# Kernel tuning notes

Measured on AMD Instinct MI355X. Metric: run time of the kernel, lower is better.

The kernel has to match this reference:

```python
import jax, jax.numpy as jnp
import numpy as np

B, S, EMBED = 8, 2048, 512
FFN = 2048
N_QUBITS = 10
DEPTH = 2


def _apply_1q(state, mats, wire):
    # state: (N,) + (2,)*n complex; mats: (N,2,2) per-token or (2,2) shared
    s = jnp.moveaxis(state, 1 + wire, 1)
    shp = s.shape
    s = s.reshape(shp[0], 2, -1)
    if mats.ndim == 3:
        s = jnp.einsum('nab,nbr->nar', mats, s)
    else:
        s = jnp.einsum('ab,nbr->nar', mats, s)
    return jnp.moveaxis(s.reshape(shp), 1, 1 + wire)


def _cnot(state, ctrl, tgt):
    # CNOT: flip target axis on the control=1 slice
    ca, ta = 1 + ctrl, 1 + tgt
    s0 = jax.lax.index_in_dim(state, 0, axis=ca, keepdims=True)
    s1 = jax.lax.index_in_dim(state, 1, axis=ca, keepdims=True)
    s1 = jnp.flip(s1, axis=ta)
    return jnp.concatenate([s0, s1], axis=ca)


def _qlayer(x_flat, theta, n_qubits=N_QUBITS, depth=DEPTH):
    # x_flat: (N, n_qubits) RX encoding angles; theta: (n_qubits,) RY params
    N = x_flat.shape[0]
    state = jnp.zeros((N,) + (2,) * n_qubits, jnp.complex64)
    state = state.at[(slice(None),) + (0,) * n_qubits].set(1.0)
    # encoder: RX(x_i) on wire i, per-token angles
    for w in range(n_qubits):
        a = x_flat[:, w] * 0.5
        c = jnp.cos(a).astype(jnp.complex64)
        s = (-1j * jnp.sin(a)).astype(jnp.complex64)
        mats = jnp.stack([jnp.stack([c, s], -1), jnp.stack([s, c], -1)], -2)  # (N,2,2)
        state = _apply_1q(state, mats, w)
    # trainable RY(theta_w) on each wire (shared across tokens)
    for w in range(n_qubits):
        a = theta[w] * 0.5
        c, s = jnp.cos(a), jnp.sin(a)
        mat = jnp.stack([jnp.stack([c, -s]), jnp.stack([s, c])]).astype(jnp.complex64)
        state = _apply_1q(state, mat, w)
    # depth rounds of ring CNOT chain
    for _ in range(depth):
        for w in range(n_qubits - 1):
            state = _cnot(state, w, w + 1)
        state = _cnot(state, n_qubits - 1, 0)
    # MeasureAll PauliZ: <Z_w> per wire
    probs = jnp.abs(state.reshape(N, -1)) ** 2  # (N, 2^n)
    bits = (jnp.arange(2 ** n_qubits)[None, :] >> (n_qubits - 1 - jnp.arange(n_qubits))[:, None]) & 1
    z = (1 - 2 * bits).astype(probs.dtype)  # (n, 2^n)
    return probs @ z.T  # (N, n)


def setup_inputs() -> dict:
    key = jax.random.key(0)
    k = jax.random.split(key, 6)
    x = jax.random.normal(k[0], (B, S, EMBED), jnp.float32)
    ry_theta = jax.random.uniform(k[1], (N_QUBITS,), jnp.float32, 0.0, 2.0 * np.pi)
    W1 = jax.random.normal(k[2], (FFN, N_QUBITS), jnp.float32) / np.sqrt(N_QUBITS)
    b1 = jax.random.normal(k[3], (FFN,), jnp.float32) * 0.01
    W2 = jax.random.normal(k[4], (EMBED, FFN), jnp.float32) / np.sqrt(FFN)
    b2 = jax.random.normal(k[5], (EMBED,), jnp.float32) * 0.01
    return {"x": x, "ry_theta": ry_theta, "W1": W1, "b1": b1, "W2": W2, "b2": b2}


def reference(x, ry_theta, W1, b1, W2, b2):
    b, s, _ = x.shape
    xf = x.reshape(b * s, -1)[:, :N_QUBITS]  # encoder only uses first n_qubits feats
    q = _qlayer(xf, ry_theta).reshape(b, s, N_QUBITS)
    # dropout is identity at eval; linear1 -> relu -> linear2
    h = jax.nn.relu(q @ W1.T + b1)
    return h @ W2.T + b2
```

## Files before the change

### kernel.cpp

```cpp
#include <hip/hip_runtime.h>
#include <hip/hip_bf16.h>


typedef __attribute__((ext_vector_type(8))) short bf16x8;
typedef __attribute__((ext_vector_type(16))) float f32x16;
typedef __attribute__((ext_vector_type(8))) unsigned short us8;
typedef unsigned int u32;

#define NTOK  16384
#define EMBED 512
#define FFN   2048
#define NQ    10
#define BM    128
#define BN    128
#define NKT   32

__device__ __forceinline__ unsigned short f2bf(float f) {
  union { float f; unsigned int u; } a; a.f = f;
  unsigned int r = a.u + 0x7FFFu + ((a.u >> 16) & 1u);
  return (unsigned short)(r >> 16);
}

__device__ __forceinline__ void gload_lds16(const void* g, void* l) {
  __builtin_amdgcn_global_load_lds(
      (const __attribute__((address_space(1))) unsigned int*)g,
      (__attribute__((address_space(3))) unsigned int*)l, 16, 0, 0);
}

__global__ __launch_bounds__(256) void k_prep(const float* __restrict__ x,
                                              const float* __restrict__ theta,
                                              const float* __restrict__ W1,
                                              const float* __restrict__ b1,
                                              const float* __restrict__ W2,
                                              unsigned short* __restrict__ W2f,
                                              unsigned short* __restrict__ W1f,
                                              unsigned short* __restrict__ Qf) {
  int bb = blockIdx.x;
  if (bb < 512) {
    int gid = bb * 256 + threadIdx.x;
    int l = gid & 63, kb = (gid >> 6) & 127, tile = gid >> 13;
    int col = tile * 32 + (l & 31);
    int k0 = kb * 16 + (l >> 5) * 8;
    const float* src = W2 + (size_t)col * FFN + k0;
    float4 v0 = *(const float4*)src;
    float4 v1 = *(const float4*)(src + 4);
    us8 o;
    o[0] = f2bf(v0.x); o[1] = f2bf(v0.y); o[2] = f2bf(v0.z); o[3] = f2bf(v0.w);
    o[4] = f2bf(v1.x); o[5] = f2bf(v1.y); o[6] = f2bf(v1.z); o[7] = f2bf(v1.w);
    *(us8*)(W2f + (size_t)gid * 8) = o;
  } else if (bb < 640) {
    int gid = (bb - 512) * 256 + threadIdx.x;
    int l = gid & 63, tile = gid >> 6;
    int tok = tile * 32 + (l & 31), g = l >> 5;
    const int masks[NQ] = {0x2AB,0x3FD,0x3FA,0x3F5,0x3EA,0x3D5,0x3AA,0x355,0x2AA,0x155};
    float z[NQ], qv[NQ];
#pragma unroll
    for (int w = 0; w < NQ; ++w)
      z[w] = __builtin_cosf(x[(size_t)tok * EMBED + w]) * __builtin_cosf(theta[w]);
#pragma unroll
    for (int w = 0; w < NQ; ++w) {
      float p = 1.f;
#pragma unroll
      for (int v = 0; v < NQ; ++v)
        if ((masks[w] >> v) & 1) p *= z[v];
      qv[w] = p;
    }
    us8 o = (us8)0;
    if (g == 0) {
#pragma unroll
      for (int e = 0; e < 8; ++e) o[e] = f2bf(qv[e]);
    } else {
      o[0] = f2bf(qv[8]); o[1] = f2bf(qv[9]); o[2] = f2bf(1.f);
    }
    *(us8*)(Qf + (size_t)gid * 8) = o;
  } else {
    int gid = (bb - 640) * 256 + threadIdx.x;
    int l = gid & 63, blk = gid >> 6;
    int k = blk * 32 + (l & 31);
    int wg = (l >> 5) * 8;
    us8 o;
#pragma unroll
    for (int e = 0; e < 8; ++e) {
      int wire = wg + e;
      float v = (wire < NQ) ? W1[k * NQ + wire] : (wire == NQ ? b1[k] : 0.f);
      o[e] = f2bf(v);
    }
    *(us8*)(W1f + (size_t)gid * 8) = o;
  }
}

__global__ __launch_bounds__(512, 4) void k_fused(const unsigned short* __restrict__ Qf,
                                                  const unsigned short* __restrict__ W1f,
                                                  const unsigned short* __restrict__ W2f,
                                                  const float* __restrict__ b2,
                                                  float* __restrict__ out) {
  __shared__ short Bw[2][16 * 64 * 8];
  __shared__ short W1s[2][2 * 64 * 8];

  int bid = blockIdx.x;
  int swz = (bid & 7) * 64 + (bid >> 3);
  const int m0 = (swz >> 2) * BM;
  const int n0 = (swz & 3) * BN;
  const int tid  = threadIdx.x;
  const int lane = tid & 63;
  const int wave = tid >> 6;
  const int wm = wave >> 1, wn = wave & 1;
  const int h = lane >> 5, t31 = lane & 31;
  const int nt0 = n0 >> 5;

  bf16x8 qf = *(const bf16x8*)&Qf[(((size_t)(m0 >> 5) + wm) * 64 + lane) * 8];

  f32x16 acc[2] = {};

#define STAGE(KT, B)                                                            \
  { _Pragma("unroll")                                                           \
    for (int hf = 0; hf < 2; ++hf) {                                            \
      int ch = hf * 512 + tid;                                                  \
      int tile2 = ch >> 8, kb = (ch >> 6) & 3, ln = ch & 63;                    \
      gload_lds16(&W2f[(((size_t)(nt0 + tile2) * 128 + (KT) * 4 + kb) * 64 + ln) * 8], \
                  &Bw[B][ch * 8]);                                              \
    }                                                                           \
    if (tid < 128)                                                              \
      gload_lds16(&W1f[(((size_t)(KT) * 2 + (tid >> 6)) * 64 + (tid & 63)) * 8],\
                  &W1s[B][tid * 8]); }

#define HGEN1(WF, AQ0, AQ1)                                                     \
  { f32x16 zz = {};                                                             \
    f32x16 d = __builtin_amdgcn_mfma_f32_32x32x16_bf16((WF), qf, zz, 0, 0, 0);  \
    u32 dw0, dw1, dw2, dw3, dw4, dw5, dw6, dw7;                                 \
    { float a0=fmaxf(d[0],0.f),a1=fmaxf(d[1],0.f);                              \
      asm("v_cvt_pk_bf16_f32 %0, %1, %2":"=v"(dw0):"v"(a0),"v"(a1)); }          \
    { float a0=fmaxf(d[2],0.f),a1=fmaxf(d[3],0.f);                              \
      asm("v_cvt_pk_bf16_f32 %0, %1, %2":"=v"(dw1):"v"(a0),"v"(a1)); }          \
    { float a0=fmaxf(d[4],0.f),a1=fmaxf(d[5],0.f);                              \
      asm("v_cvt_pk_bf16_f32 %0, %1, %2":"=v"(dw2):"v"(a0),"v"(a1)); }          \
    { float a0=fmaxf(d[6],0.f),a1=fmaxf(d[7],0.f);                              \
      asm("v_cvt_pk_bf16_f32 %0, %1, %2":"=v"(dw3):"v"(a0),"v"(a1)); }          \
    { float a0=fmaxf(d[8],0.f),a1=fmaxf(d[9],0.f);                              \
      asm("v_cvt_pk_bf16_f32 %0, %1, %2":"=v"(dw4):"v"(a0),"v"(a1)); }          \
    { float a0=fmaxf(d[10],0.f),a1=fmaxf(d[11],0.f);                            \
      asm("v_cvt_pk_bf16_f32 %0, %1, %2":"=v"(dw5):"v"(a0),"v"(a1)); }          \
    { float a0=fmaxf(d[12],0.f),a1=fmaxf(d[13],0.f);                            \
      asm("v_cvt_pk_bf16_f32 %0, %1, %2":"=v"(dw6):"v"(a0),"v"(a1)); }          \
    { float a0=fmaxf(d[14],0.f),a1=fmaxf(d[15],0.f);                            \
      asm("v_cvt_pk_bf16_f32 %0, %1, %2":"=v"(dw7):"v"(a0),"v"(a1)); }          \
    asm("v_permlane32_swap_b32 %0, %1" : "+v"(dw0), "+v"(dw2));                 \
    asm("v_permlane32_swap_b32 %0, %1" : "+v"(dw1), "+v"(dw3));                 \
    asm("v_permlane32_swap_b32 %0, %1" : "+v"(dw4), "+v"(dw6));                 \
    asm("v_permlane32_swap_b32 %0, %1" : "+v"(dw5), "+v"(dw7));                 \
    union { u32 u[4]; bf16x8 v; } u0, u1;                                       \
    u0.u[0]=dw0; u0.u[1]=dw1; u0.u[2]=dw2; u0.u[3]=dw3;                         \
    u1.u[0]=dw4; u1.u[1]=dw5; u1.u[2]=dw6; u1.u[3]=dw7;                         \
    AQ0 = u0.v; AQ1 = u1.v; }

  STAGE(0, 0);

  for (int kt = 0; kt < NKT; ++kt) {
    const int cur = kt & 1;
    asm volatile("s_waitcnt vmcnt(0)" ::: "memory");
    __builtin_amdgcn_s_barrier();
    asm volatile("" ::: "memory");
    if (kt + 1 < NKT) STAGE(kt + 1, cur ^ 1);

    bf16x8 wf0 = *(const bf16x8*)&W1s[cur][(0 * 64 + lane) * 8];
    bf16x8 wf1 = *(const bf16x8*)&W1s[cur][(1 * 64 + lane) * 8];
    bf16x8 aq00, aq01, aq10, aq11;
    HGEN1(wf0, aq00, aq01);
    HGEN1(wf1, aq10, aq11);

#pragma unroll
    for (int j = 0; j < 2; ++j) {
      bf16x8 bg0 = *(const bf16x8*)&Bw[cur][(((wn * 2 + j) * 4 + 0) * 64 + lane) * 8];
      bf16x8 bg1 = *(const bf16x8*)&Bw[cur][(((wn * 2 + j) * 4 + 1) * 64 + lane) * 8];
      bf16x8 bg2 = *(const bf16x8*)&Bw[cur][(((wn * 2 + j) * 4 + 2) * 64 + lane) * 8];
      bf16x8 bg3 = *(const bf16x8*)&Bw[cur][(((wn * 2 + j) * 4 + 3) * 64 + lane) * 8];
      __builtin_amdgcn_s_setprio(1);
      acc[j] = __builtin_amdgcn_mfma_f32_32x32x16_bf16(aq00, bg0, acc[j], 0, 0, 0);
      acc[j] = __builtin_amdgcn_mfma_f32_32x32x16_bf16(aq01, bg1, acc[j], 0, 0, 0);
      acc[j] = __builtin_amdgcn_mfma_f32_32x32x16_bf16(aq10, bg2, acc[j], 0, 0, 0);
      acc[j] = __builtin_amdgcn_mfma_f32_32x32x16_bf16(aq11, bg3, acc[j], 0, 0, 0);
      __builtin_amdgcn_s_setprio(0);
    }
  }

#pragma unroll
  for (int j = 0; j < 2; ++j) {
    const int col = n0 + wn * 64 + j * 32 + t31;
    const float bbv = b2[col];
#pragma unroll
    for (int r = 0; r < 16; ++r) {
      int tok = m0 + wm * 32 + (r & 3) + 8 * (r >> 2) + 4 * h;
      out[(size_t)tok * EMBED + col] = acc[j][r] + bbv;
    }
  }
#undef STAGE
#undef HGEN1
}

extern "C" void kernel_launch(void* const* d_in, const int* in_sizes, int n_in,
                              void* d_out, int out_size, void* d_ws, size_t ws_size,
                              hipStream_t stream) {
  const float* x     = (const float*)d_in[0];
  const float* theta = (const float*)d_in[1];
  const float* W1    = (const float*)d_in[2];
  const float* b1    = (const float*)d_in[3];
  const float* W2    = (const float*)d_in[4];
  const float* b2    = (const float*)d_in[5];
  float* out = (float*)d_out;

  char* ws = (char*)d_ws;
  unsigned short* W2f = (unsigned short*)ws;
  unsigned short* W1f = (unsigned short*)(ws + (2u << 20));
  unsigned short* Qfg = (unsigned short*)(ws + (2u << 20) + (64u << 10));

  k_prep <<<656, 256, 0, stream>>>(x, theta, W1, b1, W2, W2f, W1f, Qfg);
  k_fused<<<(NTOK / BM) * (EMBED / BN), 512, 0, stream>>>(Qfg, W1f, W2f, b2, out);
}
```

Before: 57.44 us.

## Double K-step per barrier, read W1 fragments from global, vectorize ReLU

Each LDS stage now covers two K-tiles (64 of the FFN dimension) instead of one, so barriers and waitcnt drains happen half as often, and the loop is unrolled over buffers. W1 fragments are no longer staged through LDS; each wave loads them straight from global memory, relying on cache hits. The ReLU is applied as one vector max before the bf16 packing. The cost is double the LDS footprint (64KB per block), which may reduce occupancy against the launch bound of 4 blocks, plus exposed global-load latency for W1 right after the barrier.

New measurement: 59.36 us. +3.3%, slower.

```diff
diff --git a/kernel.cpp b/kernel.cpp
--- a/kernel.cpp
+++ b/kernel.cpp
@@ -13,7 +13,7 @@
 #define NQ    10
 #define BM    128
 #define BN    128
-#define NKT   32
+#define NPAIR 16
 
 __device__ __forceinline__ unsigned short f2bf(float f) {
   union { float f; unsigned int u; } a; a.f = f;
@@ -94,8 +94,7 @@
                                                   const unsigned short* __restrict__ W2f,
                                                   const float* __restrict__ b2,
                                                   float* __restrict__ out) {
-  __shared__ short Bw[2][16 * 64 * 8];
-  __shared__ short W1s[2][2 * 64 * 8];
+  __shared__ short Bw[2][32 * 64 * 8];
 
   int bid = blockIdx.x;
   int swz = (bid & 7) * 64 + (bid >> 3);
@@ -112,38 +111,28 @@
 
   f32x16 acc[2] = {};
 
-#define STAGE(KT, B)                                                            \
+#define STAGE(P, B)                                                             \
   { _Pragma("unroll")                                                           \
-    for (int hf = 0; hf < 2; ++hf) {                                            \
+    for (int hf = 0; hf < 4; ++hf) {                                            \
       int ch = hf * 512 + tid;                                                  \
-      int tile2 = ch >> 8, kb = (ch >> 6) & 3, ln = ch & 63;                    \
-      gload_lds16(&W2f[(((size_t)(nt0 + tile2) * 128 + (KT) * 4 + kb) * 64 + ln) * 8], \
+      int tile2 = ch >> 9, kbl = (ch >> 6) & 7, ln = ch & 63;                   \
+      gload_lds16(&W2f[(((size_t)(nt0 + tile2) * 128 + (P) * 8 + kbl) * 64 + ln) * 8], \
                   &Bw[B][ch * 8]);                                              \
-    }                                                                           \
-    if (tid < 128)                                                              \
-      gload_lds16(&W1f[(((size_t)(KT) * 2 + (tid >> 6)) * 64 + (tid & 63)) * 8],\
-                  &W1s[B][tid * 8]); }
+    } }
 
 #define HGEN1(WF, AQ0, AQ1)                                                     \
   { f32x16 zz = {};                                                             \
     f32x16 d = __builtin_amdgcn_mfma_f32_32x32x16_bf16((WF), qf, zz, 0, 0, 0);  \
+    d = __builtin_elementwise_max(d, zz);                                       \
     u32 dw0, dw1, dw2, dw3, dw4, dw5, dw6, dw7;                                 \
-    { float a0=fmaxf(d[0],0.f),a1=fmaxf(d[1],0.f);                              \
-      asm("v_cvt_pk_bf16_f32 %0, %1, %2":"=v"(dw0):"v"(a0),"v"(a1)); }          \
-    { float a0=fmaxf(d[2],0.f),a1=fmaxf(d[3],0.f);                              \
-      asm("v_cvt_pk_bf16_f32 %0, %1, %2":"=v"(dw1):"v"(a0),"v"(a1)); }          \
-    { float a0=fmaxf(d[4],0.f),a1=fmaxf(d[5],0.f);                              \
-      asm("v_cvt_pk_bf16_f32 %0, %1, %2":"=v"(dw2):"v"(a0),"v"(a1)); }          \
-    { float a0=fmaxf(d[6],0.f),a1=fmaxf(d[7],0.f);                              \
-      asm("v_cvt_pk_bf16_f32 %0, %1, %2":"=v"(dw3):"v"(a0),"v"(a1)); }          \
-    { float a0=fmaxf(d[8],0.f),a1=fmaxf(d[9],0.f);                              \
-      asm("v_cvt_pk_bf16_f32 %0, %1, %2":"=v"(dw4):"v"(a0),"v"(a1)); }          \
-    { float a0=fmaxf(d[10],0.f),a1=fmaxf(d[11],0.f);                            \
-      asm("v_cvt_pk_bf16_f32 %0, %1, %2":"=v"(dw5):"v"(a0),"v"(a1)); }          \
-    { float a0=fmaxf(d[12],0.f),a1=fmaxf(d[13],0.f);                            \
-      asm("v_cvt_pk_bf16_f32 %0, %1, %2":"=v"(dw6):"v"(a0),"v"(a1)); }          \
-    { float a0=fmaxf(d[14],0.f),a1=fmaxf(d[15],0.f);                            \
-      asm("v_cvt_pk_bf16_f32 %0, %1, %2":"=v"(dw7):"v"(a0),"v"(a1)); }          \
+    asm("v_cvt_pk_bf16_f32 %0, %1, %2":"=v"(dw0):"v"(d[0]),"v"(d[1]));          \
+    asm("v_cvt_pk_bf16_f32 %0, %1, %2":"=v"(dw1):"v"(d[2]),"v"(d[3]));          \
+    asm("v_cvt_pk_bf16_f32 %0, %1, %2":"=v"(dw2):"v"(d[4]),"v"(d[5]));          \
+    asm("v_cvt_pk_bf16_f32 %0, %1, %2":"=v"(dw3):"v"(d[6]),"v"(d[7]));          \
+    asm("v_cvt_pk_bf16_f32 %0, %1, %2":"=v"(dw4):"v"(d[8]),"v"(d[9]));          \
+    asm("v_cvt_pk_bf16_f32 %0, %1, %2":"=v"(dw5):"v"(d[10]),"v"(d[11]));        \
+    asm("v_cvt_pk_bf16_f32 %0, %1, %2":"=v"(dw6):"v"(d[12]),"v"(d[13]));        \
+    asm("v_cvt_pk_bf16_f32 %0, %1, %2":"=v"(dw7):"v"(d[14]),"v"(d[15]));        \
     asm("v_permlane32_swap_b32 %0, %1" : "+v"(dw0), "+v"(dw2));                 \
     asm("v_permlane32_swap_b32 %0, %1" : "+v"(dw1), "+v"(dw3));                 \
     asm("v_permlane32_swap_b32 %0, %1" : "+v"(dw4), "+v"(dw6));                 \
@@ -153,34 +142,43 @@
     u1.u[0]=dw4; u1.u[1]=dw5; u1.u[2]=dw6; u1.u[3]=dw7;                         \
     AQ0 = u0.v; AQ1 = u1.v; }
 
+#define KTBODY(Q, B, WFA, WFB)                                                  \
+  { bf16x8 aq00, aq01, aq10, aq11;                                              \
+    HGEN1(WFA, aq00, aq01);                                                     \
+    HGEN1(WFB, aq10, aq11);                                                     \
+    _Pragma("unroll")                                                           \
+    for (int j = 0; j < 2; ++j) {                                               \
+      bf16x8 bg0 = *(const bf16x8*)&Bw[B][(((wn * 2 + j) * 8 + (Q) * 4 + 0) * 64 + lane) * 8]; \
+      bf16x8 bg1 = *(const bf16x8*)&Bw[B][(((wn * 2 + j) * 8 + (Q) * 4 + 1) * 64 + lane) * 8]; \
+      bf16x8 bg2 = *(const bf16x8*)&Bw[B][(((wn * 2 + j) * 8 + (Q) * 4 + 2) * 64 + lane) * 8]; \
+      bf16x8 bg3 = *(const bf16x8*)&Bw[B][(((wn * 2 + j) * 8 + (Q) * 4 + 3) * 64 + lane) * 8]; \
+      __builtin_amdgcn_s_setprio(1);                                            \
+      acc[j] = __builtin_amdgcn_mfma_f32_32x32x16_bf16(aq00, bg0, acc[j], 0, 0, 0); \
+      acc[j] = __builtin_amdgcn_mfma_f32_32x32x16_bf16(aq01, bg1, acc[j], 0, 0, 0); \
+      acc[j] = __builtin_amdgcn_mfma_f32_32x32x16_bf16(aq10, bg2, acc[j], 0, 0, 0); \
+      acc[j] = __builtin_amdgcn_mfma_f32_32x32x16_bf16(aq11, bg3, acc[j], 0, 0, 0); \
+      __builtin_amdgcn_s_setprio(0);                                            \
+    } }
+
+#define PAIR(P, B)                                                              \
+  {                                                                             \
+    asm volatile("s_waitcnt vmcnt(0)" ::: "memory");       \
+    __builtin_amdgcn_s_barrier();                       \
+    asm volatile("" ::: "memory");                                              \
+    bf16x8 wf0 = *(const bf16x8*)&W1f[(((size_t)(P) * 4 + 0) * 64 + lane) * 8]; \
+    bf16x8 wf1 = *(const bf16x8*)&W1f[(((size_t)(P) * 4 + 1) * 64 + lane) * 8]; \
+    bf16x8 wf2 = *(const bf16x8*)&W1f[(((size_t)(P) * 4 + 2) * 64 + lane) * 8]; \
+    bf16x8 wf3 = *(const bf16x8*)&W1f[(((size_t)(P) * 4 + 3) * 64 + lane) * 8]; \
+    if ((P) + 1 < NPAIR) STAGE((P) + 1, (B) ^ 1);                               \
+    KTBODY(0, B, wf0, wf1);                                                     \
+    KTBODY(1, B, wf2, wf3);                                                     \
+  }
+
   STAGE(0, 0);
 
-  for (int kt = 0; kt < NKT; ++kt) {
-    const int cur = kt & 1;
-    asm volatile("s_waitcnt vmcnt(0)" ::: "memory");
-    __builtin_amdgcn_s_barrier();
-    asm volatile("" ::: "memory");
-    if (kt + 1 < NKT) STAGE(kt + 1, cur ^ 1);
-
-    bf16x8 wf0 = *(const bf16x8*)&W1s[cur][(0 * 64 + lane) * 8];
-    bf16x8 wf1 = *(const bf16x8*)&W1s[cur][(1 * 64 + lane) * 8];
-    bf16x8 aq00, aq01, aq10, aq11;
-    HGEN1(wf0, aq00, aq01);
-    HGEN1(wf1, aq10, aq11);
-
-#pragma unroll
-    for (int j = 0; j < 2; ++j) {
-      bf16x8 bg0 = *(const bf16x8*)&Bw[cur][(((wn * 2 + j) * 4 + 0) * 64 + lane) * 8];
-      bf16x8 bg1 = *(const bf16x8*)&Bw[cur][(((wn * 2 + j) * 4 + 1) * 64 + lane) * 8];
-      bf16x8 bg2 = *(const bf16x8*)&Bw[cur][(((wn * 2 + j) * 4 + 2) * 64 + lane) * 8];
-      bf16x8 bg3 = *(const bf16x8*)&Bw[cur][(((wn * 2 + j) * 4 + 3) * 64 + lane) * 8];
-      __builtin_amdgcn_s_setprio(1);
-      acc[j] = __builtin_amdgcn_mfma_f32_32x32x16_bf16(aq00, bg0, acc[j], 0, 0, 0);
-      acc[j] = __builtin_amdgcn_mfma_f32_32x32x16_bf16(aq01, bg1, acc[j], 0, 0, 0);
-      acc[j] = __builtin_amdgcn_mfma_f32_32x32x16_bf16(aq10, bg2, acc[j], 0, 0, 0);
-      acc[j] = __builtin_amdgcn_mfma_f32_32x32x16_bf16(aq11, bg3, acc[j], 0, 0, 0);
-      __builtin_amdgcn_s_setprio(0);
-    }
+  for (int p2 = 0; p2 < NPAIR / 2; ++p2) {
+    PAIR(2 * p2,     0);
+    PAIR(2 * p2 + 1, 1);
   }
 
 #pragma unroll
@@ -195,6 +193,8 @@
   }
 #undef STAGE
 #undef HGEN1
+#undef KTBODY
+#undef PAIR
 }
 
 extern "C" void kernel_launch(void* const* d_in, const int* in_sizes, int n_in,
```

## Halve block N-tile and workgroup size, interleave MFMA accumulators

Applied to the files above, without the earlier changes.

Shrinks the N tile from 128 to 64 and the workgroup from 8 to 4 waves, so each wave covers one 32-row M slice and both 32-column N subtiles. The grid doubles to 1024 blocks, giving more parallelism and smaller LDS per block. The MFMA chain interleaves two independent accumulators to hide dependency latency, drops the setprio hints, and applies ReLU as a single vector max. The tradeoff is more blocks each loading their own W1/W2 slices, and hidden-layer generation repeated across more n-tiles.

New measurement: 55.67 us, median of 3. -3.1%, faster.

```diff
diff --git a/kernel.cpp b/kernel.cpp
--- a/kernel.cpp
+++ b/kernel.cpp
@@ -12,7 +12,7 @@
 #define FFN   2048
 #define NQ    10
 #define BM    128
-#define BN    128
+#define BN    64
 #define NKT   32
 
 __device__ __forceinline__ unsigned short f2bf(float f) {
@@ -89,33 +89,32 @@
   }
 }
 
-__global__ __launch_bounds__(512, 4) void k_fused(const unsigned short* __restrict__ Qf,
+__global__ __launch_bounds__(256, 4) void k_fused(const unsigned short* __restrict__ Qf,
                                                   const unsigned short* __restrict__ W1f,
                                                   const unsigned short* __restrict__ W2f,
                                                   const float* __restrict__ b2,
                                                   float* __restrict__ out) {
-  __shared__ short Bw[2][16 * 64 * 8];
+  __shared__ short Bw[2][8 * 64 * 8];
   __shared__ short W1s[2][2 * 64 * 8];
 
   int bid = blockIdx.x;
-  int swz = (bid & 7) * 64 + (bid >> 3);
-  const int m0 = (swz >> 2) * BM;
-  const int n0 = (swz & 3) * BN;
+  int swz = (bid & 7) * 128 + (bid >> 3);
+  const int m0 = (swz >> 3) * BM;
+  const int n0 = (swz & 7) * BN;
   const int tid  = threadIdx.x;
   const int lane = tid & 63;
   const int wave = tid >> 6;
-  const int wm = wave >> 1, wn = wave & 1;
   const int h = lane >> 5, t31 = lane & 31;
   const int nt0 = n0 >> 5;
 
-  bf16x8 qf = *(const bf16x8*)&Qf[(((size_t)(m0 >> 5) + wm) * 64 + lane) * 8];
+  bf16x8 qf = *(const bf16x8*)&Qf[(((size_t)(m0 >> 5) + wave) * 64 + lane) * 8];
 
   f32x16 acc[2] = {};
 
 #define STAGE(KT, B)                                                            \
   { _Pragma("unroll")                                                           \
     for (int hf = 0; hf < 2; ++hf) {                                            \
-      int ch = hf * 512 + tid;                                                  \
+      int ch = hf * 256 + tid;                                                  \
       int tile2 = ch >> 8, kb = (ch >> 6) & 3, ln = ch & 63;                    \
       gload_lds16(&W2f[(((size_t)(nt0 + tile2) * 128 + (KT) * 4 + kb) * 64 + ln) * 8], \
                   &Bw[B][ch * 8]);                                              \
@@ -127,23 +126,16 @@
 #define HGEN1(WF, AQ0, AQ1)                                                     \
   { f32x16 zz = {};                                                             \
     f32x16 d = __builtin_amdgcn_mfma_f32_32x32x16_bf16((WF), qf, zz, 0, 0, 0);  \
+    d = __builtin_elementwise_max(d, zz);                                       \
     u32 dw0, dw1, dw2, dw3, dw4, dw5, dw6, dw7;                                 \
-    { float a0=fmaxf(d[0],0.f),a1=fmaxf(d[1],0.f);                              \
-      asm("v_cvt_pk_bf16_f32 %0, %1, %2":"=v"(dw0):"v"(a0),"v"(a1)); }          \
-    { float a0=fmaxf(d[2],0.f),a1=fmaxf(d[3],0.f);                              \
-      asm("v_cvt_pk_bf16_f32 %0, %1, %2":"=v"(dw1):"v"(a0),"v"(a1)); }          \
-    { float a0=fmaxf(d[4],0.f),a1=fmaxf(d[5],0.f);                              \
-      asm("v_cvt_pk_bf16_f32 %0, %1, %2":"=v"(dw2):"v"(a0),"v"(a1)); }          \
-    { float a0=fmaxf(d[6],0.f),a1=fmaxf(d[7],0.f);                              \
-      asm("v_cvt_pk_bf16_f32 %0, %1, %2":"=v"(dw3):"v"(a0),"v"(a1)); }          \
-    { float a0=fmaxf(d[8],0.f),a1=fmaxf(d[9],0.f);                              \
-      asm("v_cvt_pk_bf16_f32 %0, %1, %2":"=v"(dw4):"v"(a0),"v"(a1)); }          \
-    { float a0=fmaxf(d[10],0.f),a1=fmaxf(d[11],0.f);                            \
-      asm("v_cvt_pk_bf16_f32 %0, %1, %2":"=v"(dw5):"v"(a0),"v"(a1)); }          \
-    { float a0=fmaxf(d[12],0.f),a1=fmaxf(d[13],0.f);                            \
-      asm("v_cvt_pk_bf16_f32 %0, %1, %2":"=v"(dw6):"v"(a0),"v"(a1)); }          \
-    { float a0=fmaxf(d[14],0.f),a1=fmaxf(d[15],0.f);                            \
-      asm("v_cvt_pk_bf16_f32 %0, %1, %2":"=v"(dw7):"v"(a0),"v"(a1)); }          \
+    asm("v_cvt_pk_bf16_f32 %0, %1, %2":"=v"(dw0):"v"(d[0]),"v"(d[1]));          \
+    asm("v_cvt_pk_bf16_f32 %0, %1, %2":"=v"(dw1):"v"(d[2]),"v"(d[3]));          \
+    asm("v_cvt_pk_bf16_f32 %0, %1, %2":"=v"(dw2):"v"(d[4]),"v"(d[5]));          \
+    asm("v_cvt_pk_bf16_f32 %0, %1, %2":"=v"(dw3):"v"(d[6]),"v"(d[7]));          \
+    asm("v_cvt_pk_bf16_f32 %0, %1, %2":"=v"(dw4):"v"(d[8]),"v"(d[9]));          \
+    asm("v_cvt_pk_bf16_f32 %0, %1, %2":"=v"(dw5):"v"(d[10]),"v"(d[11]));        \
+    asm("v_cvt_pk_bf16_f32 %0, %1, %2":"=v"(dw6):"v"(d[12]),"v"(d[13]));        \
+    asm("v_cvt_pk_bf16_f32 %0, %1, %2":"=v"(dw7):"v"(d[14]),"v"(d[15]));        \
     asm("v_permlane32_swap_b32 %0, %1" : "+v"(dw0), "+v"(dw2));                 \
     asm("v_permlane32_swap_b32 %0, %1" : "+v"(dw1), "+v"(dw3));                 \
     asm("v_permlane32_swap_b32 %0, %1" : "+v"(dw4), "+v"(dw6));                 \
@@ -164,32 +156,35 @@
 
     bf16x8 wf0 = *(const bf16x8*)&W1s[cur][(0 * 64 + lane) * 8];
     bf16x8 wf1 = *(const bf16x8*)&W1s[cur][(1 * 64 + lane) * 8];
-    bf16x8 aq00, aq01, aq10, aq11;
-    HGEN1(wf0, aq00, aq01);
-    HGEN1(wf1, aq10, aq11);
-
-#pragma unroll
-    for (int j = 0; j < 2; ++j) {
-      bf16x8 bg0 = *(const bf16x8*)&Bw[cur][(((wn * 2 + j) * 4 + 0) * 64 + lane) * 8];
-      bf16x8 bg1 = *(const bf16x8*)&Bw[cur][(((wn * 2 + j) * 4 + 1) * 64 + lane) * 8];
-      bf16x8 bg2 = *(const bf16x8*)&Bw[cur][(((wn * 2 + j) * 4 + 2) * 64 + lane) * 8];
-      bf16x8 bg3 = *(const bf16x8*)&Bw[cur][(((wn * 2 + j) * 4 + 3) * 64 + lane) * 8];
-      __builtin_amdgcn_s_setprio(1);
-      acc[j] = __builtin_amdgcn_mfma_f32_32x32x16_bf16(aq00, bg0, acc[j], 0, 0, 0);
-      acc[j] = __builtin_amdgcn_mfma_f32_32x32x16_bf16(aq01, bg1, acc[j], 0, 0, 0);
-      acc[j] = __builtin_amdgcn_mfma_f32_32x32x16_bf16(aq10, bg2, acc[j], 0, 0, 0);
-      acc[j] = __builtin_amdgcn_mfma_f32_32x32x16_bf16(aq11, bg3, acc[j], 0, 0, 0);
-      __builtin_amdgcn_s_setprio(0);
-    }
+    bf16x8 aq0, aq1, aq2, aq3;
+    HGEN1(wf0, aq0, aq1);
+    HGEN1(wf1, aq2, aq3);
+
+    bf16x8 bg00 = *(const bf16x8*)&Bw[cur][((0 * 4 + 0) * 64 + lane) * 8];
+    bf16x8 bg01 = *(const bf16x8*)&Bw[cur][((0 * 4 + 1) * 64 + lane) * 8];
+    bf16x8 bg02 = *(const bf16x8*)&Bw[cur][((0 * 4 + 2) * 64 + lane) * 8];
+    bf16x8 bg03 = *(const bf16x8*)&Bw[cur][((0 * 4 + 3) * 64 + lane) * 8];
+    bf16x8 bg10 = *(const bf16x8*)&Bw[cur][((1 * 4 + 0) * 64 + lane) * 8];
+    bf16x8 bg11 = *(const bf16x8*)&Bw[cur][((1 * 4 + 1) * 64 + lane) * 8];
+    bf16x8 bg12 = *(const bf16x8*)&Bw[cur][((1 * 4 + 2) * 64 + lane) * 8];
+    bf16x8 bg13 = *(const bf16x8*)&Bw[cur][((1 * 4 + 3) * 64 + lane) * 8];
+    acc[0] = __builtin_amdgcn_mfma_f32_32x32x16_bf16(aq0, bg00, acc[0], 0, 0, 0);
+    acc[1] = __builtin_amdgcn_mfma_f32_32x32x16_bf16(aq0, bg10, acc[1], 0, 0, 0);
+    acc[0] = __builtin_amdgcn_mfma_f32_32x32x16_bf16(aq1, bg01, acc[0], 0, 0, 0);
+    acc[1] = __builtin_amdgcn_mfma_f32_32x32x16_bf16(aq1, bg11, acc[1], 0, 0, 0);
+    acc[0] = __builtin_amdgcn_mfma_f32_32x32x16_bf16(aq2, bg02, acc[0], 0, 0, 0);
+    acc[1] = __builtin_amdgcn_mfma_f32_32x32x16_bf16(aq2, bg12, acc[1], 0, 0, 0);
+    acc[0] = __builtin_amdgcn_mfma_f32_32x32x16_bf16(aq3, bg03, acc[0], 0, 0, 0);
+    acc[1] = __builtin_amdgcn_mfma_f32_32x32x16_bf16(aq3, bg13, acc[1], 0, 0, 0);
   }
 
 #pragma unroll
   for (int j = 0; j < 2; ++j) {
-    const int col = n0 + wn * 64 + j * 32 + t31;
+    const int col = n0 + j * 32 + t31;
     const float bbv = b2[col];
 #pragma unroll
     for (int r = 0; r < 16; ++r) {
-      int tok = m0 + wm * 32 + (r & 3) + 8 * (r >> 2) + 4 * h;
+      int tok = m0 + wave * 32 + (r & 3) + 8 * (r >> 2) + 4 * h;
       out[(size_t)tok * EMBED + col] = acc[j][r] + bbv;
     }
   }
@@ -214,5 +209,5 @@
   unsigned short* Qfg = (unsigned short*)(ws + (2u << 20) + (64u << 10));
 
   k_prep <<<656, 256, 0, stream>>>(x, theta, W1, b1, W2, W2f, W1f, Qfg);
-  k_fused<<<(NTOK / BM) * (EMBED / BN), 512, 0, stream>>>(Qfg, W1f, W2f, b2, out);
-}
+  k_fused<<<(NTOK / BM) * (EMBED / BN), 256, 0, stream>>>(Qfg, W1f, W2f, b2, out);
+}
```
